# Kernel optimization log

Measured on AMD Instinct MI355X. Metric: run time of the kernel, lower is better.

Reference implementation:

```python
import jax, jax.numpy as jnp
import numpy as np

DIM = 512
NUM_HEADS = 8
HEAD_DIM = DIM // NUM_HEADS
SCALE = HEAD_DIM ** -0.5


def setup_inputs() -> dict:
    key = jax.random.key(0)
    k1, k2, k3, k4 = jax.random.split(key, 4)
    x = jax.random.normal(k1, (4, 2048, DIM), dtype=jnp.float32)
    W_qkv = jax.random.normal(k2, (DIM, 3 * DIM), dtype=jnp.float32) * (DIM ** -0.5)
    W_proj = jax.random.normal(k3, (DIM, DIM), dtype=jnp.float32) * (DIM ** -0.5)
    b_proj = jax.random.normal(k4, (DIM,), dtype=jnp.float32) * 0.01
    return {"x": x, "W_qkv": W_qkv, "W_proj": W_proj, "b_proj": b_proj}


def reference(x, W_qkv, W_proj, b_proj):
    B, N, C = x.shape
    H, hd = NUM_HEADS, HEAD_DIM
    # qkv: [B, N, 3, H, hd] -> (q, k, v) each [B, H, N, hd]
    qkv = (x @ W_qkv).reshape(B, N, 3, H, hd)
    qkv = jnp.transpose(qkv, (2, 0, 3, 1, 4))
    q, k, v = qkv[0], qkv[1], qkv[2]
    # eager attention: [B, H, N, N]
    attn = jnp.einsum('bhnd,bhmd->bhnm', q, k) * SCALE
    attn = jax.nn.softmax(attn, axis=-1)
    out = jnp.einsum('bhnm,bhmd->bhnd', attn, v)  # [B, H, N, hd]
    out = jnp.transpose(out, (0, 2, 1, 3)).reshape(B, N, C)
    out = out @ W_proj + b_proj
    return (out, k, v)
```

## Files before the change

### kernel.cpp

```cpp
#include <hip/hip_runtime.h>

typedef unsigned short ushort_t;
typedef __bf16 bf16x8 __attribute__((ext_vector_type(8)));
typedef ushort_t u16x8 __attribute__((ext_vector_type(8)));
typedef float f32x4 __attribute__((ext_vector_type(4)));

#define MFMA(a, b, c) __builtin_amdgcn_mfma_f32_16x16x32_bf16(a, b, c, 0, 0, 0)

#define N_X      4194304L
#define OUT_OFF_K 4194304L
#define OUT_OFF_V 8388608L

#define OFF_XB     1024UL
#define OFF_WQKVT  (OFF_XB + 8388608UL)
#define OFF_WPROJT (OFF_WQKVT + 1572864UL)
#define OFF_BPROJ  (OFF_WPROJT + 524288UL)
#define OFF_QB     (OFF_BPROJ + 2048UL)
#define OFF_KB     (OFF_QB + 8388608UL)
#define OFF_VTB    (OFF_KB + 8388608UL)
#define OFF_ATTN   (OFF_VTB + 8388608UL)

#define QSCALE 0.180336880519191f

__device__ __forceinline__ ushort_t f2b(float f) {
    union { float f; unsigned u; } v; v.f = f;
    return (ushort_t)((v.u + 0x7FFFu + ((v.u >> 16) & 1u)) >> 16);
}
__device__ __forceinline__ float b2f(ushort_t h) {
    union { unsigned u; float f; } v; v.u = ((unsigned)h) << 16;
    return v.f;
}

__device__ __forceinline__ float fast_exp2(float x) {
#if __has_builtin(__builtin_amdgcn_exp2f)
    return __builtin_amdgcn_exp2f(x);
#else
    return __expf(x * 0.6931471805599453f);
#endif
}

__device__ __forceinline__ void glds16(const void* g, const void* l) {
    __builtin_amdgcn_global_load_lds((__attribute__((address_space(1))) void*)g,
                                     (__attribute__((address_space(3))) void*)l,
                                     16, 0, 0);
}

__device__ __forceinline__ int detect_bf16(const unsigned* __restrict__ x) {
    int lane = threadIdx.x & 63;
    int cnt = 0;
#pragma unroll
    for (int i = 0; i < 4; ++i) {
        unsigned w = x[lane + i * 64];
        float v = __uint_as_float((w & 0xFFFFu) << 16);
        float a = fabsf(v);
        if (a > 1e-3f && a < 100.0f) cnt++;
    }
#pragma unroll
    for (int off = 1; off < 64; off <<= 1) cnt += __shfl_xor(cnt, off, 64);
    return cnt > 128;
}

__global__ __launch_bounds__(256)
void k_prep(const void* __restrict__ xv, const void* __restrict__ wqv,
            const void* __restrict__ wpv, const void* __restrict__ bpv,
            ushort_t* __restrict__ xb, ushort_t* __restrict__ wqT,
            ushort_t* __restrict__ wpT, float* __restrict__ bpf) {
    const int isb = detect_bf16((const unsigned*)xv);
    const int bid = blockIdx.x, tid = threadIdx.x;
    if (bid < 256) {
        __shared__ ushort_t T[64 * 64];
        int t = bid;
        const void* src; ushort_t* dst; int ncols, tr, tc;
        if (t < 192) { tr = t / 24; tc = t % 24; src = wqv; dst = wqT; ncols = 1536; }
        else { t -= 192; tr = t >> 3; tc = t & 7; src = wpv; dst = wpT; ncols = 512; }
        const int k0 = tr * 64, n0 = tc * 64;
        const int row = tid >> 2, cq = tid & 3;
        if (isb) {
            const ushort_t* s = (const ushort_t*)src;
#pragma unroll
            for (int half = 0; half < 2; ++half) {
                int c = cq + half * 4;
                u16x8 v = *(const u16x8*)(s + (long)(k0 + row) * ncols + n0 + c * 8);
#pragma unroll
                for (int e = 0; e < 8; ++e) {
                    int nl = c * 8 + e;
                    T[row * 64 + ((nl + row) & 63)] = v[e];
                }
            }
        } else {
            const float* s = (const float*)src;
#pragma unroll
            for (int half = 0; half < 2; ++half) {
                int c = cq + half * 4;
                f32x4 a = *(const f32x4*)(s + (long)(k0 + row) * ncols + n0 + c * 8);
                f32x4 b = *(const f32x4*)(s + (long)(k0 + row) * ncols + n0 + c * 8 + 4);
#pragma unroll
                for (int e = 0; e < 4; ++e) {
                    T[row * 64 + ((c * 8 + e + row) & 63)] = f2b(a[e]);
                    T[row * 64 + ((c * 8 + 4 + e + row) & 63)] = f2b(b[e]);
                }
            }
        }
        __syncthreads();
#pragma unroll
        for (int it = 0; it < 16; ++it) {
            int nrow = (tid >> 6) * 16 + it;
            int kcol = tid & 63;
            dst[(long)(n0 + nrow) * 512 + k0 + kcol] = T[kcol * 64 + ((nrow + kcol) & 63)];
        }
    } else {
        long i0 = (long)(bid - 256) * 256 + tid;
        long stride = (long)(gridDim.x - 256) * 256;
        if (isb) {
            const u16x8* x = (const u16x8*)xv;
            for (long i = i0; i < N_X / 8; i += stride) ((u16x8*)xb)[i] = x[i];
            const ushort_t* bp = (const ushort_t*)bpv;
            for (long i = i0; i < 512; i += stride) bpf[i] = b2f(bp[i]);
        } else {
            const f32x4* x = (const f32x4*)xv;
            for (long i = i0; i < N_X / 8; i += stride) {
                f32x4 a = x[i * 2], b = x[i * 2 + 1];
                u16x8 o;
#pragma unroll
                for (int e = 0; e < 4; ++e) { o[e] = f2b(a[e]); o[e + 4] = f2b(b[e]); }
                ((u16x8*)xb)[i] = o;
            }
            const float* bp = (const float*)bpv;
            for (long i = i0; i < 512; i += stride) bpf[i] = bp[i];
        }
    }
}

__global__ __launch_bounds__(256, 4)
void k_qkv(const unsigned* __restrict__ xraw,
           const ushort_t* __restrict__ xb, const ushort_t* __restrict__ wqT,
           ushort_t* __restrict__ qb, ushort_t* __restrict__ kb, ushort_t* __restrict__ vtb,
           void* __restrict__ dout) {
    const int isb = detect_bf16(xraw);
    __shared__ __align__(16) ushort_t As[128 * 64];
    __shared__ __align__(16) ushort_t Bs[128 * 64];
    const int tid = threadIdx.x, wave = tid >> 6, lane = tid & 63;
    const int id = blockIdx.x;
    const int xcd = id & 7, g = id >> 3;
    const int bx = xcd * 8 + (g & 7);
    const int by = g >> 3;
    const int tm = bx * 128, tn = by * 128;
    const int wm = (wave >> 1) * 64, wn = (wave & 1) * 64;
    const int l15 = lane & 15, lq = lane >> 4;
    const int srow = lane >> 3, schunk = lane & 7;

    f32x4 acc[4][4];
#pragma unroll
    for (int a = 0; a < 4; ++a)
#pragma unroll
        for (int b = 0; b < 4; ++b) acc[a][b] = (f32x4){0.f, 0.f, 0.f, 0.f};

    for (int k0 = 0; k0 < 512; k0 += 64) {
#pragma unroll
        for (int t = 0; t < 4; ++t) {
            int s = wave * 4 + t;
            int row = s * 8 + srow;
            int c = schunk ^ (row & 7);
            glds16(xb  + (long)(tm + row) * 512 + k0 + c * 8, As + s * 512);
            glds16(wqT + (long)(tn + row) * 512 + k0 + c * 8, Bs + s * 512);
        }
        __syncthreads();
#pragma unroll
        for (int kt = 0; kt < 2; ++kt) {
            bf16x8 af[4], bfr[4];
#pragma unroll
            for (int mt = 0; mt < 4; ++mt) {
                int row = wm + mt * 16 + l15;
                int c = (kt * 4 + lq) ^ (row & 7);
                af[mt] = *(const bf16x8*)(As + row * 64 + c * 8);
            }
#pragma unroll
            for (int nt = 0; nt < 4; ++nt) {
                int row = wn + nt * 16 + l15;
                int c = (kt * 4 + lq) ^ (row & 7);
                bfr[nt] = *(const bf16x8*)(Bs + row * 64 + c * 8);
            }
#pragma unroll
            for (int mt = 0; mt < 4; ++mt)
#pragma unroll
                for (int nt = 0; nt < 4; ++nt)
                    acc[mt][nt] = MFMA(af[mt], bfr[nt], acc[mt][nt]);
        }
        __syncthreads();
    }

    float*    koutf = (float*)dout + OUT_OFF_K;
    float*    voutf = (float*)dout + OUT_OFF_V;
    ushort_t* koutb = (ushort_t*)dout + OUT_OFF_K;
    ushort_t* voutb = (ushort_t*)dout + OUT_OFF_V;
#pragma unroll
    for (int mt = 0; mt < 4; ++mt) {
#pragma unroll
        for (int nt = 0; nt < 4; ++nt) {
            int j = tn + wn + nt * 16 + l15;
            int t = j >> 9, h = (j >> 6) & 7, d = j & 63;
            int mm0 = tm + wm + mt * 16 + lq * 4;
            int b = mm0 >> 11, nn0 = mm0 & 2047;
            long base = ((long)(b * 8 + h) * 2048 + nn0) * 64 + d;
            if (t == 0) {
#pragma unroll
                for (int r = 0; r < 4; ++r)
                    qb[base + (long)r * 64] = f2b(acc[mt][nt][r] * QSCALE);
            } else if (t == 1) {
#pragma unroll
                for (int r = 0; r < 4; ++r) {
                    float v = acc[mt][nt][r];
                    kb[base + (long)r * 64] = f2b(v);
                    if (isb) koutb[base + (long)r * 64] = f2b(v);
                    else     koutf[base + (long)r * 64] = v;
                }
            } else {
                union { ushort_t u[4]; unsigned long long ll; } o;
#pragma unroll
                for (int r = 0; r < 4; ++r) {
                    float v = acc[mt][nt][r];
                    o.u[r] = f2b(v);
                    if (isb) voutb[base + (long)r * 64] = f2b(v);
                    else     voutf[base + (long)r * 64] = v;
                }
                *(unsigned long long*)(vtb + ((long)(b * 8 + h) * 64 + d) * 2048 + nn0) = o.ll;
            }
        }
    }
}

__global__ __launch_bounds__(256, 2)
void k_attn(const ushort_t* __restrict__ qb, const ushort_t* __restrict__ kb,
            const ushort_t* __restrict__ vtb, ushort_t* __restrict__ attnb) {
    __shared__ __align__(16) ushort_t Kt[2][128 * 64];
    __shared__ __align__(16) ushort_t Vt[2][64 * 128];
    const int tid = threadIdx.x, wave = tid >> 6, lane = tid & 63;
    const int l15 = lane & 15, lq = lane >> 4;
    const int id = blockIdx.x;
    const int xcd = id & 7, g = id >> 3;
    const int bh = xcd * 4 + (g >> 4);
    const int qt = g & 15;
    const long kvbase = (long)bh * 131072;
    const long qbase = kvbase + (long)qt * 128 * 64;

    const int ksrow = lane >> 3, kschunk = lane & 7;
    const int vsrow = lane >> 4, vschunk = lane & 15;

    auto stage = [&](int j, int buf) {
#pragma unroll
        for (int t = 0; t < 4; ++t) {
            int s = wave * 4 + t;
            {
                int p = s * 8 + ksrow;
                int pos = p & 15;
                int akey = ((p >> 5) << 5) + ((pos >> 2) << 3) + (pos & 3) + ((p >> 4) & 1) * 4;
                int c = kschunk ^ (p & 7);
                glds16(kb + kvbase + (long)(j * 128 + akey) * 64 + c * 8, &Kt[buf][s * 512]);
            }
            {
                int row = s * 4 + vsrow;
                int c = vschunk ^ (row & 15);
                glds16(vtb + kvbase + (long)row * 2048 + j * 128 + c * 8, &Vt[buf][s * 512]);
            }
        }
    };

    stage(0, 0);

    bf16x8 aQ[2][2];
#pragma unroll
    for (int mq = 0; mq < 2; ++mq)
#pragma unroll
        for (int kt = 0; kt < 2; ++kt)
            aQ[mq][kt] = *(const bf16x8*)(qb + qbase +
                (long)(wave * 32 + mq * 16 + l15) * 64 + kt * 32 + lq * 8);

    union { ushort_t u[8]; bf16x8 v; } oneu;
#pragma unroll
    for (int i = 0; i < 8; ++i) oneu.u[i] = 0x3F80;
    const bf16x8 ones8 = oneu.v;

    f32x4 oacc[2][4], sum_acc[2];
#pragma unroll
    for (int mq = 0; mq < 2; ++mq) {
#pragma unroll
        for (int nd = 0; nd < 4; ++nd) oacc[mq][nd] = (f32x4){0.f, 0.f, 0.f, 0.f};
        sum_acc[mq] = (f32x4){0.f, 0.f, 0.f, 0.f};
    }

    for (int j = 0; j < 16; ++j) {
        int cur = j & 1;
        if (j < 15) {
            stage(j + 1, cur ^ 1);
            asm volatile("s_waitcnt vmcnt(8)" ::: "memory");
        } else {
            asm volatile("s_waitcnt vmcnt(0)" ::: "memory");
        }
        __builtin_amdgcn_sched_barrier(0);
        __builtin_amdgcn_s_barrier();

        const ushort_t* Ktc = &Kt[cur][0];
        const ushort_t* Vtc = &Vt[cur][0];

        f32x4 sacc[2][8];
#pragma unroll
        for (int mq = 0; mq < 2; ++mq)
#pragma unroll
            for (int nt = 0; nt < 8; ++nt) sacc[mq][nt] = (f32x4){0.f, 0.f, 0.f, 0.f};
#pragma unroll
        for (int nt = 0; nt < 8; ++nt) {
            int krow = nt * 16 + l15;
#pragma unroll
            for (int kt = 0; kt < 2; ++kt) {
                int c = (kt * 4 + lq) ^ (krow & 7);
                bf16x8 bk = *(const bf16x8*)(Ktc + krow * 64 + c * 8);
                sacc[0][nt] = MFMA(bk, aQ[0][kt], sacc[0][nt]);
                sacc[1][nt] = MFMA(bk, aQ[1][kt], sacc[1][nt]);
            }
        }

        bf16x8 pb8[2][4];
#pragma unroll
        for (int mq = 0; mq < 2; ++mq)
#pragma unroll
            for (int nt = 0; nt < 8; ++nt)
#pragma unroll
                for (int r = 0; r < 4; ++r)
                    pb8[mq][nt >> 1][(nt & 1) * 4 + r] =
                        (__bf16)fast_exp2(sacc[mq][nt][r]);

#pragma unroll
        for (int t = 0; t < 4; ++t) {
            sum_acc[0] = MFMA(ones8, pb8[0][t], sum_acc[0]);
            sum_acc[1] = MFMA(ones8, pb8[1][t], sum_acc[1]);
#pragma unroll
            for (int nd = 0; nd < 4; ++nd) {
                int drow = nd * 16 + l15;
                int cc = (t * 4 + lq) ^ (drow & 15);
                bf16x8 va = *(const bf16x8*)(Vtc + drow * 128 + cc * 8);
                oacc[0][nd] = MFMA(va, pb8[0][t], oacc[0][nd]);
                oacc[1][nd] = MFMA(va, pb8[1][t], oacc[1][nd]);
            }
        }

        asm volatile("s_waitcnt lgkmcnt(0)" ::: "memory");
        __builtin_amdgcn_sched_barrier(0);
        __builtin_amdgcn_s_barrier();
    }

    const int b = bh >> 3, hh = bh & 7;
#pragma unroll
    for (int mq = 0; mq < 2; ++mq) {
        float inv = 1.0f / sum_acc[mq][0];
        int n = qt * 128 + wave * 32 + mq * 16 + l15;
        long rowbase = ((long)b * 2048 + n) * 512 + hh * 64;
#pragma unroll
        for (int nd = 0; nd < 4; ++nd) {
            int d0 = nd * 16 + lq * 4;
            union { ushort_t u[4]; unsigned long long ll; } o;
#pragma unroll
            for (int r = 0; r < 4; ++r) o.u[r] = f2b(oacc[mq][nd][r] * inv);
            *(unsigned long long*)(attnb + rowbase + d0) = o.ll;
        }
    }
}

__global__ __launch_bounds__(256, 2)
void k_proj(const unsigned* __restrict__ xraw,
            const ushort_t* __restrict__ ab, const ushort_t* __restrict__ wpT,
            const float* __restrict__ bpf, void* __restrict__ dout) {
    const int isb = detect_bf16(xraw);
    __shared__ __align__(16) ushort_t As[64 * 32];
    __shared__ __align__(16) ushort_t Bs[128 * 32];
    const int tid = threadIdx.x, wave = tid >> 6, lane = tid & 63;
    const int id = blockIdx.x;
    const int xcd = id & 7, g = id >> 3;
    const int bx = xcd * 16 + (g & 15);
    const int by = g >> 4;
    const int tm = bx * 64, tn = by * 128;
    const int wm = (wave >> 1) * 32, wn = (wave & 1) * 64;
    const int l15 = lane & 15, lq = lane >> 4;
    const int srow = lane >> 2, sc = lane & 3;

    f32x4 acc[2][4];
#pragma unroll
    for (int a = 0; a < 2; ++a)
#pragma unroll
        for (int b = 0; b < 4; ++b) acc[a][b] = (f32x4){0.f, 0.f, 0.f, 0.f};

    for (int k0 = 0; k0 < 512; k0 += 32) {
        {
            int s = wave;
            int row = s * 16 + srow;
            int c = (sc ^ (row >> 1)) & 3;
            glds16(ab + (long)(tm + row) * 512 + k0 + c * 8, As + s * 512);
        }
#pragma unroll
        for (int t = 0; t < 2; ++t) {
            int s = wave * 2 + t;
            int row = s * 16 + srow;
            int c = (sc ^ (row >> 1)) & 3;
            glds16(wpT + (long)(tn + row) * 512 + k0 + c * 8, Bs + s * 512);
        }
        __syncthreads();
        bf16x8 af[2], bfr[4];
#pragma unroll
        for (int mt = 0; mt < 2; ++mt) {
            int row = wm + mt * 16 + l15;
            int cp = (lq ^ (row >> 1)) & 3;
            af[mt] = *(const bf16x8*)(As + row * 32 + cp * 8);
        }
#pragma unroll
        for (int nt = 0; nt < 4; ++nt) {
            int row = wn + nt * 16 + l15;
            int cp = (lq ^ (row >> 1)) & 3;
            bfr[nt] = *(const bf16x8*)(Bs + row * 32 + cp * 8);
        }
#pragma unroll
        for (int mt = 0; mt < 2; ++mt)
#pragma unroll
            for (int nt = 0; nt < 4; ++nt)
                acc[mt][nt] = MFMA(af[mt], bfr[nt], acc[mt][nt]);
        __syncthreads();
    }

#pragma unroll
    for (int mt = 0; mt < 2; ++mt) {
#pragma unroll
        for (int nt = 0; nt < 4; ++nt) {
            int j = tn + wn + nt * 16 + l15;
            float bias = bpf[j];
#pragma unroll
            for (int r = 0; r < 4; ++r) {
                int mm = tm + wm + mt * 16 + lq * 4 + r;
                float v = acc[mt][nt][r] + bias;
                if (isb) ((ushort_t*)dout)[(long)mm * 512 + j] = f2b(v);
                else     ((float*)dout)[(long)mm * 512 + j] = v;
            }
        }
    }
}

extern "C" void kernel_launch(void* const* d_in, const int* in_sizes, int n_in,
                              void* d_out, int out_size, void* d_ws, size_t ws_size,
                              hipStream_t stream) {
    (void)in_sizes; (void)n_in; (void)out_size; (void)ws_size;
    char* ws = (char*)d_ws;
    ushort_t* xb  = (ushort_t*)(ws + OFF_XB);
    ushort_t* wqT = (ushort_t*)(ws + OFF_WQKVT);
    ushort_t* wpT = (ushort_t*)(ws + OFF_WPROJT);
    float*    bpf = (float*)(ws + OFF_BPROJ);
    ushort_t* qb  = (ushort_t*)(ws + OFF_QB);
    ushort_t* kb  = (ushort_t*)(ws + OFF_KB);
    ushort_t* vtb = (ushort_t*)(ws + OFF_VTB);
    ushort_t* ab  = (ushort_t*)(ws + OFF_ATTN);

    k_prep<<<1280, 256, 0, stream>>>(d_in[0], d_in[1], d_in[2], d_in[3],
                                     xb, wqT, wpT, bpf);

    k_qkv<<<768, 256, 0, stream>>>((const unsigned*)d_in[0], xb, wqT,
                                   qb, kb, vtb, d_out);

    k_attn<<<512, 256, 0, stream>>>(qb, kb, vtb, ab);

    k_proj<<<512, 256, 0, stream>>>((const unsigned*)d_in[0], ab, wpT, bpf, d_out);
}
```

Before: 151.0 us.

## Split attention over key halves with partial outputs and a combine kernel

Each attention block now processes only half of the key sequence, which doubles the grid to 1024 blocks. Partial fp32 outputs and softmax denominators go to workspace, and a new combine kernel sums them and normalizes into bf16. LDS double buffering is dropped in favour of single buffers with __syncthreads so that four blocks fit per CU, and s_setprio raises wave priority around the MFMA sections. The cost is extra global traffic for the fp32 partials, an additional kernel launch, and no more overlap between loads and compute inside a block.

```diff
diff --git a/kernel.cpp b/kernel.cpp
--- a/kernel.cpp
+++ b/kernel.cpp
@@ -19,6 +19,8 @@
 #define OFF_KB     (OFF_QB + 8388608UL)
 #define OFF_VTB    (OFF_KB + 8388608UL)
 #define OFF_ATTN   (OFF_VTB + 8388608UL)
+#define OFF_OPART  (OFF_ATTN + 8388608UL)
+#define OFF_DPART  (OFF_OPART + 33554432UL)
 
 #define QSCALE 0.180336880519191f
 
@@ -229,24 +231,27 @@
     }
 }
 
-__global__ __launch_bounds__(256, 2)
+__global__ __launch_bounds__(256, 4)
 void k_attn(const ushort_t* __restrict__ qb, const ushort_t* __restrict__ kb,
-            const ushort_t* __restrict__ vtb, ushort_t* __restrict__ attnb) {
-    __shared__ __align__(16) ushort_t Kt[2][128 * 64];
-    __shared__ __align__(16) ushort_t Vt[2][64 * 128];
+            const ushort_t* __restrict__ vtb,
+            float* __restrict__ opart, float* __restrict__ dpart) {
+    __shared__ __align__(16) ushort_t Kt[128 * 64];
+    __shared__ __align__(16) ushort_t Vt[64 * 128];
     const int tid = threadIdx.x, wave = tid >> 6, lane = tid & 63;
     const int l15 = lane & 15, lq = lane >> 4;
     const int id = blockIdx.x;
     const int xcd = id & 7, g = id >> 3;
-    const int bh = xcd * 4 + (g >> 4);
+    const int bh = xcd * 4 + (g >> 5);
+    const int half = (g >> 4) & 1;
     const int qt = g & 15;
     const long kvbase = (long)bh * 131072;
     const long qbase = kvbase + (long)qt * 128 * 64;
+    const int koff = half * 1024;
 
     const int ksrow = lane >> 3, kschunk = lane & 7;
     const int vsrow = lane >> 4, vschunk = lane & 15;
 
-    auto stage = [&](int j, int buf) {
+    auto stage = [&](int j) {
 #pragma unroll
         for (int t = 0; t < 4; ++t) {
             int s = wave * 4 + t;
@@ -255,17 +260,15 @@
                 int pos = p & 15;
                 int akey = ((p >> 5) << 5) + ((pos >> 2) << 3) + (pos & 3) + ((p >> 4) & 1) * 4;
                 int c = kschunk ^ (p & 7);
-                glds16(kb + kvbase + (long)(j * 128 + akey) * 64 + c * 8, &Kt[buf][s * 512]);
+                glds16(kb + kvbase + (long)(koff + j * 128 + akey) * 64 + c * 8, Kt + s * 512);
             }
             {
                 int row = s * 4 + vsrow;
                 int c = vschunk ^ (row & 15);
-                glds16(vtb + kvbase + (long)row * 2048 + j * 128 + c * 8, &Vt[buf][s * 512]);
+                glds16(vtb + kvbase + (long)row * 2048 + koff + j * 128 + c * 8, Vt + s * 512);
             }
         }
     };
-
-    stage(0, 0);
 
     bf16x8 aQ[2][2];
 #pragma unroll
@@ -288,81 +291,93 @@
         sum_acc[mq] = (f32x4){0.f, 0.f, 0.f, 0.f};
     }
 
-    for (int j = 0; j < 16; ++j) {
-        int cur = j & 1;
-        if (j < 15) {
-            stage(j + 1, cur ^ 1);
-            asm volatile("s_waitcnt vmcnt(8)" ::: "memory");
-        } else {
-            asm volatile("s_waitcnt vmcnt(0)" ::: "memory");
-        }
-        __builtin_amdgcn_sched_barrier(0);
-        __builtin_amdgcn_s_barrier();
-
-        const ushort_t* Ktc = &Kt[cur][0];
-        const ushort_t* Vtc = &Vt[cur][0];
-
-        f32x4 sacc[2][8];
-#pragma unroll
-        for (int mq = 0; mq < 2; ++mq)
-#pragma unroll
-            for (int nt = 0; nt < 8; ++nt) sacc[mq][nt] = (f32x4){0.f, 0.f, 0.f, 0.f};
-#pragma unroll
-        for (int nt = 0; nt < 8; ++nt) {
-            int krow = nt * 16 + l15;
-#pragma unroll
-            for (int kt = 0; kt < 2; ++kt) {
-                int c = (kt * 4 + lq) ^ (krow & 7);
-                bf16x8 bk = *(const bf16x8*)(Ktc + krow * 64 + c * 8);
-                sacc[0][nt] = MFMA(bk, aQ[0][kt], sacc[0][nt]);
-                sacc[1][nt] = MFMA(bk, aQ[1][kt], sacc[1][nt]);
-            }
-        }
-
-        bf16x8 pb8[2][4];
-#pragma unroll
-        for (int mq = 0; mq < 2; ++mq)
-#pragma unroll
-            for (int nt = 0; nt < 8; ++nt)
-#pragma unroll
-                for (int r = 0; r < 4; ++r)
-                    pb8[mq][nt >> 1][(nt & 1) * 4 + r] =
-                        (__bf16)fast_exp2(sacc[mq][nt][r]);
-
-#pragma unroll
-        for (int t = 0; t < 4; ++t) {
-            sum_acc[0] = MFMA(ones8, pb8[0][t], sum_acc[0]);
-            sum_acc[1] = MFMA(ones8, pb8[1][t], sum_acc[1]);
-#pragma unroll
-            for (int nd = 0; nd < 4; ++nd) {
-                int drow = nd * 16 + l15;
-                int cc = (t * 4 + lq) ^ (drow & 15);
-                bf16x8 va = *(const bf16x8*)(Vtc + drow * 128 + cc * 8);
-                oacc[0][nd] = MFMA(va, pb8[0][t], oacc[0][nd]);
-                oacc[1][nd] = MFMA(va, pb8[1][t], oacc[1][nd]);
-            }
-        }
-
-        asm volatile("s_waitcnt lgkmcnt(0)" ::: "memory");
-        __builtin_amdgcn_sched_barrier(0);
-        __builtin_amdgcn_s_barrier();
-    }
-
+    for (int j = 0; j < 8; ++j) {
+        stage(j);
+        __syncthreads();
+
+#pragma unroll
+        for (int h = 0; h < 2; ++h) {
+            f32x4 sacc[2][4];
+#pragma unroll
+            for (int mq = 0; mq < 2; ++mq)
+#pragma unroll
+                for (int nt = 0; nt < 4; ++nt) sacc[mq][nt] = (f32x4){0.f, 0.f, 0.f, 0.f};
+            __builtin_amdgcn_s_setprio(1);
+#pragma unroll
+            for (int nt = 0; nt < 4; ++nt) {
+                int krow = h * 64 + nt * 16 + l15;
+#pragma unroll
+                for (int kt = 0; kt < 2; ++kt) {
+                    int c = (kt * 4 + lq) ^ (krow & 7);
+                    bf16x8 bk = *(const bf16x8*)(Kt + krow * 64 + c * 8);
+                    sacc[0][nt] = MFMA(bk, aQ[0][kt], sacc[0][nt]);
+                    sacc[1][nt] = MFMA(bk, aQ[1][kt], sacc[1][nt]);
+                }
+            }
+            __builtin_amdgcn_s_setprio(0);
+
+            bf16x8 pb8[2][2];
+#pragma unroll
+            for (int mq = 0; mq < 2; ++mq)
+#pragma unroll
+                for (int nt = 0; nt < 4; ++nt)
+#pragma unroll
+                    for (int r = 0; r < 4; ++r)
+                        pb8[mq][nt >> 1][(nt & 1) * 4 + r] =
+                            (__bf16)fast_exp2(sacc[mq][nt][r]);
+
+            __builtin_amdgcn_s_setprio(1);
+#pragma unroll
+            for (int t = 0; t < 2; ++t) {
+                int tt = h * 2 + t;
+                sum_acc[0] = MFMA(ones8, pb8[0][t], sum_acc[0]);
+                sum_acc[1] = MFMA(ones8, pb8[1][t], sum_acc[1]);
+#pragma unroll
+                for (int nd = 0; nd < 4; ++nd) {
+                    int drow = nd * 16 + l15;
+                    int cc = (tt * 4 + lq) ^ (drow & 15);
+                    bf16x8 va = *(const bf16x8*)(Vt + drow * 128 + cc * 8);
+                    oacc[0][nd] = MFMA(va, pb8[0][t], oacc[0][nd]);
+                    oacc[1][nd] = MFMA(va, pb8[1][t], oacc[1][nd]);
+                }
+            }
+            __builtin_amdgcn_s_setprio(0);
+        }
+        __syncthreads();
+    }
+
+#pragma unroll
+    for (int mq = 0; mq < 2; ++mq) {
+        int n = qt * 128 + wave * 32 + mq * 16 + l15;
+        long obase = ((long)(half * 32 + bh) * 2048 + n) * 64;
+#pragma unroll
+        for (int nd = 0; nd < 4; ++nd)
+            *(f32x4*)(opart + obase + nd * 16 + lq * 4) = oacc[mq][nd];
+        if (lq == 0) dpart[(long)(half * 32 + bh) * 2048 + n] = sum_acc[mq][0];
+    }
+}
+
+__global__ __launch_bounds__(256, 8)
+void k_comb(const float* __restrict__ opart, const float* __restrict__ dpart,
+            ushort_t* __restrict__ attnb) {
+    const int tid = threadIdx.x;
+    const int id = blockIdx.x;
+    const int xcd = id & 7, g = id >> 3;
+    const int bh = xcd * 4 + (g >> 7);
+    const int nblk = g & 127;
+    const int n = nblk * 16 + (tid >> 4);
+    const int d0 = (tid & 15) * 4;
+    long o1 = ((long)bh * 2048 + n) * 64 + d0;
+    long o2 = ((long)(32 + bh) * 2048 + n) * 64 + d0;
+    f32x4 a = *(const f32x4*)(opart + o1);
+    f32x4 c = *(const f32x4*)(opart + o2);
+    float den = dpart[(long)bh * 2048 + n] + dpart[(long)(32 + bh) * 2048 + n];
+    float inv = 1.0f / den;
     const int b = bh >> 3, hh = bh & 7;
-#pragma unroll
-    for (int mq = 0; mq < 2; ++mq) {
-        float inv = 1.0f / sum_acc[mq][0];
-        int n = qt * 128 + wave * 32 + mq * 16 + l15;
-        long rowbase = ((long)b * 2048 + n) * 512 + hh * 64;
-#pragma unroll
-        for (int nd = 0; nd < 4; ++nd) {
-            int d0 = nd * 16 + lq * 4;
-            union { ushort_t u[4]; unsigned long long ll; } o;
-#pragma unroll
-            for (int r = 0; r < 4; ++r) o.u[r] = f2b(oacc[mq][nd][r] * inv);
-            *(unsigned long long*)(attnb + rowbase + d0) = o.ll;
-        }
-    }
+    union { ushort_t u[4]; unsigned long long ll; } o;
+#pragma unroll
+    for (int r = 0; r < 4; ++r) o.u[r] = f2b((a[r] + c[r]) * inv);
+    *(unsigned long long*)(attnb + ((long)b * 2048 + n) * 512 + hh * 64 + d0) = o.ll;
 }
 
 __global__ __launch_bounds__(256, 2)
@@ -454,6 +469,8 @@
     ushort_t* kb  = (ushort_t*)(ws + OFF_KB);
     ushort_t* vtb = (ushort_t*)(ws + OFF_VTB);
     ushort_t* ab  = (ushort_t*)(ws + OFF_ATTN);
+    float*    opart = (float*)(ws + OFF_OPART);
+    float*    dpart = (float*)(ws + OFF_DPART);
 
     k_prep<<<1280, 256, 0, stream>>>(d_in[0], d_in[1], d_in[2], d_in[3],
                                      xb, wqT, wpT, bpf);
@@ -461,7 +478,9 @@
     k_qkv<<<768, 256, 0, stream>>>((const unsigned*)d_in[0], xb, wqT,
                                    qb, kb, vtb, d_out);
 
-    k_attn<<<512, 256, 0, stream>>>(qb, kb, vtb, ab);
+    k_attn<<<1024, 256, 0, stream>>>(qb, kb, vtb, opart, dpart);
+
+    k_comb<<<4096, 256, 0, stream>>>(opart, dpart, ab);
 
     k_proj<<<512, 256, 0, stream>>>((const unsigned*)d_in[0], ab, wpT, bpf, d_out);
 }
```

Measured after the change: 161.5 us. 6.9% more time.
